# Optimization experiments

Hardware: AMD Instinct MI355X
Metric: run time of the kernel (lower is better)

The kernel has to match this reference:

```python
import jax, jax.numpy as jnp
import numpy as np

IN_FEATURES = 4096
OUT_FEATURES = 11008
BATCH, SEQ = 8, 16


def setup_inputs() -> dict:
    key = jax.random.key(0)
    k_in, k_w, k_s, k_b = jax.random.split(key, 4)
    inp = jax.random.normal(k_in, (BATCH, SEQ, IN_FEATURES), dtype=jnp.float32)
    # int8 weights in [-128, 127], as torch.randint(-128, 127, ...)
    quantized_weights = jax.random.randint(
        k_w, (OUT_FEATURES, IN_FEATURES), -128, 127, dtype=jnp.int32
    ).astype(jnp.int8)
    scales = jax.random.normal(k_s, (OUT_FEATURES,), dtype=jnp.float32)
    bias = jax.random.normal(k_b, (1, OUT_FEATURES), dtype=jnp.float32)
    return {"input": inp, "quantized_weights": quantized_weights,
            "scales": scales, "bias": bias}


def reference(input, quantized_weights, scales, bias):
    # dequantize weight to activation dtype, then linear: y = x @ W^T
    w = quantized_weights.astype(input.dtype)  # [O, I]
    out = jnp.einsum("bsi,oi->bso", input, w)  # [B, S, O]
    out = out * scales  # per-output-channel scale
    out = out + bias    # bias shape [1, O] broadcasts
    return out
```

## Files before the change

kernel.cpp:

```cpp
#include <hip/hip_runtime.h>
#include <stdint.h>


#define M_ROWS 128
#define K_DIM  4096
#define N_DIM  11008
#define CHUNKS 64
#define NT64   (N_DIM / 64)
#define XP_BYTES (M_ROWS * K_DIM * 2)

typedef __attribute__((ext_vector_type(8))) short bf16x8;
typedef __attribute__((ext_vector_type(4))) float f32x4;
typedef const unsigned __attribute__((address_space(1)))* gas1_t;
typedef unsigned __attribute__((address_space(3)))* las3_t;

__device__ __forceinline__ unsigned bf16_rn(float f) {
  unsigned u = __float_as_uint(f);
  return (u + 0x7FFFu + ((u >> 16) & 1u)) >> 16;
}
__device__ __forceinline__ unsigned pk2(int a, int b) {
  unsigned lo = __float_as_uint((float)a), hi = __float_as_uint((float)b);
#if __has_builtin(__builtin_amdgcn_perm)
  return __builtin_amdgcn_perm(hi, lo, 0x07060302u);
#else
  return (hi & 0xFFFF0000u) | (lo >> 16);
#endif
}

__device__ __forceinline__ void gload_lds16(const void* g, void* lds) {
#if __has_builtin(__builtin_amdgcn_global_load_lds)
  __builtin_amdgcn_global_load_lds((gas1_t)g, (las3_t)(size_t)(unsigned)(size_t)lds,
                                   16, 0, 0);
#else
  *(uint4*)lds = *(const uint4*)g;
#endif
}

#define BAR()    asm volatile("s_barrier" ::: "memory")
#define WBAR16() asm volatile("s_waitcnt vmcnt(16)\n\ts_barrier" ::: "memory")
#define WBAR8()  asm volatile("s_waitcnt vmcnt(8)\n\ts_barrier" ::: "memory")
#define WBAR0()  asm volatile("s_waitcnt vmcnt(0)\n\ts_barrier" ::: "memory")

__global__ __launch_bounds__(256) void pack_x_kernel(
    const float* __restrict__ x, unsigned short* __restrict__ xp) {
  int tid  = blockIdx.x * 256 + threadIdx.x;
  int lane = tid & 63;
  int h    = (tid >> 6) & 1;
  int mf   = (tid >> 7) & 7;
  int kk   = tid >> 10;
  int m     = mf * 16 + (lane & 15);
  int kbase = kk * 64 + h * 32 + ((lane >> 4) * 8);
  const float* src = x + (size_t)m * K_DIM + kbase;
  float4 f0 = *(const float4*)(src);
  float4 f1 = *(const float4*)(src + 4);
  float v[8] = {f0.x, f0.y, f0.z, f0.w, f1.x, f1.y, f1.z, f1.w};
  unsigned po[4];
#pragma unroll
  for (int i = 0; i < 4; ++i)
    po[i] = bf16_rn(v[2 * i]) | (bf16_rn(v[2 * i + 1]) << 16);
  *(uint4*)(xp + (size_t)tid * 8) = *(uint4*)po;
}

struct BReg { uint4 v[4]; };

__global__ __launch_bounds__(256, 1) void gemm4w_kernel(
    const unsigned short* __restrict__ xp,
    const int* __restrict__ wq,
    const float* __restrict__ scales,
    const float* __restrict__ bias,
    float* __restrict__ out) {
  __shared__ char As[4 * 16384];

  const int tid  = threadIdx.x;
  const int lane = tid & 63;
  const int w    = tid >> 6;
  const int nt   = blockIdx.x;
  const size_t n0 = (size_t)nt * 64 + (size_t)w * 16;
  const int l15 = lane & 15, lh = lane >> 4;

  const char* agp = (const char*)xp + tid * 16;
  const int* bptr = wq + (n0 + (size_t)l15) * K_DIM + lh * 8;

  f32x4 acc[8];
  {
    f32x4 z = {0.f, 0.f, 0.f, 0.f};
#pragma unroll
    for (int i = 0; i < 8; ++i) acc[i] = z;
  }

  auto STAGE = [&](int t, int bufOff) {
#pragma unroll
    for (int i = 0; i < 4; ++i)
      gload_lds16(agp + (size_t)t * 16384 + (size_t)i * 4096,
                  As + bufOff + tid * 16 + i * 4096);
  };
  auto LOADB = [&](int t, BReg& R) {
    const int* bp = bptr + t * 64;
    R.v[0] = *(const uint4*)(bp);
    R.v[1] = *(const uint4*)(bp + 4);
    R.v[2] = *(const uint4*)(bp + 32);
    R.v[3] = *(const uint4*)(bp + 36);
  };
  auto COMP = [&](const char* ab, BReg& R) {
    bf16x8 cv[2];
#pragma unroll
    for (int s = 0; s < 2; ++s) {
      union { unsigned u[4]; bf16x8 b; } c;
      c.u[0] = pk2((int)R.v[s * 2].x,     (int)R.v[s * 2].y);
      c.u[1] = pk2((int)R.v[s * 2].z,     (int)R.v[s * 2].w);
      c.u[2] = pk2((int)R.v[s * 2 + 1].x, (int)R.v[s * 2 + 1].y);
      c.u[3] = pk2((int)R.v[s * 2 + 1].z, (int)R.v[s * 2 + 1].w);
      cv[s] = c.b;
    }
#pragma unroll
    for (int mf = 0; mf < 8; ++mf)
#pragma unroll
      for (int s = 0; s < 2; ++s) {
        bf16x8 a = *(const bf16x8*)(ab + (mf * 2 + s) * 1024 + lane * 16);
        acc[mf] = __builtin_amdgcn_mfma_f32_16x16x32_bf16(a, cv[s], acc[mf], 0, 0, 0);
      }
  };

#define PHASE(T, RCUR, RNXT)                       \
    LOADB((T) + 2, RNXT);                          \
    BAR();                                         \
    STAGE((T) + 2, (((T) + 2) & 3) * 16384);       \
    WBAR16();                                      \
    COMP(As + ((T) & 3) * 16384, RCUR);

  BReg R0, R1, R2, R3;
  STAGE(0, 0);
  LOADB(0, R0);
  STAGE(1, 16384);
  LOADB(1, R1);

#pragma unroll 1
  for (int t = 0; t < CHUNKS - 4; t += 4) {
    PHASE(t + 0, R0, R2);
    PHASE(t + 1, R1, R3);
    PHASE(t + 2, R2, R0);
    PHASE(t + 3, R3, R1);
  }
  PHASE(CHUNKS - 4, R0, R2);
  PHASE(CHUNKS - 3, R1, R3);
  WBAR8();
  COMP(As + 2 * 16384, R2);
  WBAR0();
  COMP(As + 3 * 16384, R3);
#undef PHASE

  const size_t n = n0 + (size_t)l15;
  const float sc = scales[n], bi = bias[n];
#pragma unroll
  for (int mf = 0; mf < 8; ++mf) {
    const int mb = mf * 16 + lh * 4;
#pragma unroll
    for (int r = 0; r < 4; ++r)
      out[(size_t)(mb + r) * N_DIM + n] = sc * acc[mf][r] + bi;
  }
}

__global__ __launch_bounds__(256) void naive_kernel(
    const float* __restrict__ x, const int* __restrict__ wq,
    const float* __restrict__ scales, const float* __restrict__ bias,
    float* __restrict__ out) {
  const int n = blockIdx.x * 256 + threadIdx.x;
  const int m = blockIdx.y;
  const float* xr = x + (size_t)m * K_DIM;
  const int* wr = wq + (size_t)n * K_DIM;
  float s = 0.f;
  for (int k = 0; k < K_DIM; k += 4) {
    float4 xv = *(const float4*)(xr + k);
    int4  wv = *(const int4*)(wr + k);
    s += xv.x * (float)wv.x + xv.y * (float)wv.y +
         xv.z * (float)wv.z + xv.w * (float)wv.w;
  }
  out[(size_t)m * N_DIM + n] = scales[n] * s + bias[n];
}

extern "C" void kernel_launch(void* const* d_in, const int* in_sizes, int n_in,
                              void* d_out, int out_size, void* d_ws, size_t ws_size,
                              hipStream_t stream) {
  const float* x      = (const float*)d_in[0];
  const int* wq       = (const int*)d_in[1];
  const float* scales = (const float*)d_in[2];
  const float* bias   = (const float*)d_in[3];
  float* out          = (float*)d_out;

  if (ws_size < (size_t)XP_BYTES) {
    naive_kernel<<<dim3(N_DIM / 256, M_ROWS), 256, 0, stream>>>(x, wq, scales, bias, out);
    return;
  }
  unsigned short* xp = (unsigned short*)d_ws;

  pack_x_kernel<<<256, 256, 0, stream>>>(x, xp);
  gemm4w_kernel<<<dim3(NT64), 256, 0, stream>>>(xp, wq, scales, bias, out);
}
```

Measured before the change: 64.32 us.

## Split K across four blocks with partial-sum buffers and separate reduce kernel

New measurement: 52.55 us. -18.3%, faster.

```diff
diff --git a/kernel.cpp b/kernel.cpp
--- a/kernel.cpp
+++ b/kernel.cpp
@@ -7,7 +7,10 @@
 #define N_DIM  11008
 #define CHUNKS 64
 #define NT64   (N_DIM / 64)
+#define KSPLIT 4
+#define CPB    (CHUNKS / KSPLIT)
 #define XP_BYTES (M_ROWS * K_DIM * 2)
+#define PART_ELEMS ((size_t)M_ROWS * (size_t)N_DIM)
 
 typedef __attribute__((ext_vector_type(8))) short bf16x8;
 typedef __attribute__((ext_vector_type(4))) float f32x4;
@@ -63,23 +66,23 @@
 
 struct BReg { uint4 v[4]; };
 
-__global__ __launch_bounds__(256, 1) void gemm4w_kernel(
+__global__ __launch_bounds__(256, 3) void gemm4w_kernel(
     const unsigned short* __restrict__ xp,
     const int* __restrict__ wq,
-    const float* __restrict__ scales,
-    const float* __restrict__ bias,
-    float* __restrict__ out) {
-  __shared__ char As[4 * 16384];
+    float* __restrict__ part) {
+  __shared__ char As[3 * 16384];
 
   const int tid  = threadIdx.x;
   const int lane = tid & 63;
   const int w    = tid >> 6;
   const int nt   = blockIdx.x;
+  const int kz   = blockIdx.y;
+  const int kk0  = kz * CPB;
   const size_t n0 = (size_t)nt * 64 + (size_t)w * 16;
   const int l15 = lane & 15, lh = lane >> 4;
 
-  const char* agp = (const char*)xp + tid * 16;
-  const int* bptr = wq + (n0 + (size_t)l15) * K_DIM + lh * 8;
+  const char* agp = (const char*)xp + (size_t)kk0 * 16384 + tid * 16;
+  const int* bptr = wq + (n0 + (size_t)l15) * K_DIM + (size_t)kk0 * 64 + lh * 8;
 
   f32x4 acc[8];
   {
@@ -121,43 +124,65 @@
       }
   };
 
-#define PHASE(T, RCUR, RNXT)                       \
-    LOADB((T) + 2, RNXT);                          \
-    BAR();                                         \
-    STAGE((T) + 2, (((T) + 2) & 3) * 16384);       \
-    WBAR16();                                      \
-    COMP(As + ((T) & 3) * 16384, RCUR);
-
-  BReg R0, R1, R2, R3;
+#define PHASE(T, CBUF, NBUF, RC, RN)              \
+    LOADB((T) + 2, RN);                           \
+    BAR();                                        \
+    STAGE((T) + 2, (NBUF) * 16384);               \
+    WBAR16();                                     \
+    COMP(As + (CBUF) * 16384, RC);
+
+  BReg R0, R1, R2;
   STAGE(0, 0);
   LOADB(0, R0);
   STAGE(1, 16384);
   LOADB(1, R1);
 
 #pragma unroll 1
-  for (int t = 0; t < CHUNKS - 4; t += 4) {
-    PHASE(t + 0, R0, R2);
-    PHASE(t + 1, R1, R3);
-    PHASE(t + 2, R2, R0);
-    PHASE(t + 3, R3, R1);
-  }
-  PHASE(CHUNKS - 4, R0, R2);
-  PHASE(CHUNKS - 3, R1, R3);
+  for (int t = 0; t < 12; t += 3) {
+    PHASE(t + 0, 0, 2, R0, R2);
+    PHASE(t + 1, 1, 0, R1, R0);
+    PHASE(t + 2, 2, 1, R2, R1);
+  }
+  PHASE(12, 0, 2, R0, R2);
+  PHASE(13, 1, 0, R1, R0);
   WBAR8();
   COMP(As + 2 * 16384, R2);
   WBAR0();
-  COMP(As + 3 * 16384, R3);
+  COMP(As + 0 * 16384, R0);
 #undef PHASE
 
-  const size_t n = n0 + (size_t)l15;
-  const float sc = scales[n], bi = bias[n];
+  float* pb = part + (size_t)kz * PART_ELEMS + n0 + l15;
 #pragma unroll
   for (int mf = 0; mf < 8; ++mf) {
     const int mb = mf * 16 + lh * 4;
 #pragma unroll
     for (int r = 0; r < 4; ++r)
-      out[(size_t)(mb + r) * N_DIM + n] = sc * acc[mf][r] + bi;
-  }
+      pb[(size_t)(mb + r) * N_DIM] = acc[mf][r];
+  }
+}
+
+__global__ __launch_bounds__(256) void reduce_kernel(
+    const float* __restrict__ part, const float* __restrict__ scales,
+    const float* __restrict__ bias, float* __restrict__ out) {
+  const int m = blockIdx.y;
+  const int c4 = blockIdx.x * 256 + threadIdx.x;
+  if (c4 >= N_DIM / 4) return;
+  const size_t n = (size_t)c4 * 4;
+  const float* p = part + (size_t)m * N_DIM + n;
+  float4 s = *(const float4*)(p);
+#pragma unroll
+  for (int z = 1; z < KSPLIT; ++z) {
+    float4 q = *(const float4*)(p + (size_t)z * PART_ELEMS);
+    s.x += q.x; s.y += q.y; s.z += q.z; s.w += q.w;
+  }
+  float4 sc = *(const float4*)(scales + n);
+  float4 bi = *(const float4*)(bias + n);
+  float4 r;
+  r.x = sc.x * s.x + bi.x;
+  r.y = sc.y * s.y + bi.y;
+  r.z = sc.z * s.z + bi.z;
+  r.w = sc.w * s.w + bi.w;
+  *(float4*)(out + (size_t)m * N_DIM + n) = r;
 }
 
 __global__ __launch_bounds__(256) void naive_kernel(
@@ -187,12 +212,16 @@
   const float* bias   = (const float*)d_in[3];
   float* out          = (float*)d_out;
 
-  if (ws_size < (size_t)XP_BYTES) {
+  const size_t need = (size_t)XP_BYTES + KSPLIT * PART_ELEMS * sizeof(float);
+  if (ws_size < need) {
     naive_kernel<<<dim3(N_DIM / 256, M_ROWS), 256, 0, stream>>>(x, wq, scales, bias, out);
     return;
   }
   unsigned short* xp = (unsigned short*)d_ws;
+  float* part        = (float*)((char*)d_ws + XP_BYTES);
 
   pack_x_kernel<<<256, 256, 0, stream>>>(x, xp);
-  gemm4w_kernel<<<dim3(NT64), 256, 0, stream>>>(xp, wq, scales, bias, out);
-}
+  gemm4w_kernel<<<dim3(NT64, KSPLIT), 256, 0, stream>>>(xp, wq, part);
+  reduce_kernel<<<dim3((N_DIM / 4 + 255) / 256, M_ROWS), 256, 0, stream>>>(
+      part, scales, bias, out);
+}
```
